# Performance work log

Measured on AMD Instinct MI355X. Metric: run time of the kernel, lower is better.

## Reference

```python
import jax, jax.numpy as jnp
import numpy as np

# SuperposedExpert: K parallel TT-factorized FFN paths + holographic routing.
# d_model=1024 factorized as [32,32]; d_ff=4096 as [64,64]; tt_ranks=[1,16,1] (r0/r2 squeezed).
K, D_MODEL, D_FF, RANK = 4, 1024, 4096, 16
IN1, IN2 = 32, 32          # factorize_for_tt(d_model)
F1, F2 = 64, 64            # factorize_for_tt(d_ff)
TEMP = 1.0                 # routing_temperature


def setup_inputs() -> dict:
    key = jax.random.key(0)
    ks = jax.random.split(key, 8)
    s = 0.05
    tokens = jax.random.normal(ks[0], (2048, D_MODEL), dtype=jnp.float32)
    # TT cores for ffn1: d_model -> d_ff  (input_dims [32,32], output_dims [64,64])
    ffn1_core1 = jax.random.normal(ks[1], (K, IN1, F1, RANK), dtype=jnp.float32) * s
    ffn1_core2 = jax.random.normal(ks[2], (K, RANK, IN2, F2), dtype=jnp.float32) * s
    # TT cores for ffn2: d_ff -> d_model (input_dims [64,64], output_dims [32,32])
    ffn2_core1 = jax.random.normal(ks[3], (K, F1, IN1, RANK), dtype=jnp.float32) * s
    ffn2_core2 = jax.random.normal(ks[4], (K, RANK, F2, IN2), dtype=jnp.float32) * s
    # Holographic routing params (hd_dim == d_model -> identity HD projection)
    pb = jax.random.normal(ks[5], (K, D_MODEL), dtype=jnp.float32)
    path_bases = pb / jnp.linalg.norm(pb, axis=-1, keepdims=True)  # orthogonal-ish init
    path_weights = jax.random.normal(ks[6], (K, D_MODEL), dtype=jnp.float32) * s
    return {
        'tokens': tokens,
        'ffn1_core1': ffn1_core1, 'ffn1_core2': ffn1_core2,
        'ffn2_core1': ffn2_core1, 'ffn2_core2': ffn2_core2,
        'path_bases': path_bases, 'path_weights': path_weights,
    }


def reference(tokens, ffn1_core1, ffn1_core2, ffn2_core1, ffn2_core2,
              path_bases, path_weights):
    N = tokens.shape[0]
    # ---- K superposed TT-FFN paths ----
    x3 = tokens.reshape(N, IN1, IN2)  # [n, a, b]
    # TT matmul 1: y[x,y] = sum_{a,b,r} G1[a,x,r] G2[r,b,y] x[a,b]
    h = jnp.einsum('nab,kaxr,krby->knxy', x3, ffn1_core1, ffn1_core2)
    h = jax.nn.gelu(h.reshape(K, N, D_FF))  # quantum_activation stand-in
    h3 = h.reshape(K, N, F1, F2)
    y = jnp.einsum('knab,kaxr,krby->knxy', h3, ffn2_core1, ffn2_core2)
    y = y.reshape(K, N, D_MODEL)  # per-path outputs
    # ---- Holographic HD routing (hd_dim == d_model: identity projection) ----
    logits = jnp.einsum('nd,kd->nk', tokens, path_bases) / TEMP
    gates = jax.nn.softmax(logits, axis=-1)  # [n, k]
    # Collapse superposition: per-path elementwise HD modulation + gated sum
    out = jnp.einsum('knd,kd,nk->nd', y, 1.0 + path_weights, gates)
    return out
```

## Files before the change

### kernel.cpp

```cpp
#include <hip/hip_runtime.h>
#include <stdint.h>

#define GAS __attribute__((address_space(1)))
#define LAS __attribute__((address_space(3)))

typedef __attribute__((ext_vector_type(8))) short short8;
typedef __attribute__((ext_vector_type(16))) float f32x16;
typedef __attribute__((ext_vector_type(4))) float f32x4;

static constexpr int N_TOK = 2048;
static constexpr int DM    = 1024;
static constexpr int DF    = 4096;
static constexpr int KP    = 4;

__device__ inline unsigned short f2bf(float f) {
  union { float f; uint32_t u; } v; v.f = f;
  uint32_t u = v.u;
  u += 0x7FFFu + ((u >> 16) & 1u);
  return (unsigned short)(u >> 16);
}

__device__ inline uint32_t pk_bf(float lo, float hi) {
  union { float f; uint32_t u; } a, b; a.f = lo; b.f = hi;
  uint32_t ul = a.u + 0x7FFFu + ((a.u >> 16) & 1u);
  uint32_t uh = b.u + 0x7FFFu + ((b.u >> 16) & 1u);
  return (ul >> 16) | (uh & 0xFFFF0000u);
}

__device__ inline float gelu_gate(float v, float g) {
  float t0 = v * v;
  float u  = v * __builtin_fmaf(t0, -0.10294456f, -2.3022539f);
  float e  = __builtin_amdgcn_exp2f(u);
  float r  = __builtin_amdgcn_rcpf(1.0f + e);
  return v * g * r;
}

__device__ inline void gld16(const void* g, void* l) {
  __builtin_amdgcn_global_load_lds((const GAS void*)g, (LAS void*)l, 16, 0, 0);
}

__global__ __launch_bounds__(256) void setup_kernel(
    const float* __restrict__ tokens, const float* __restrict__ pb,
    const float* __restrict__ c11, const float* __restrict__ c12,
    const float* __restrict__ c21, const float* __restrict__ c22,
    float* __restrict__ gates, unsigned short* __restrict__ xb,
    unsigned short* __restrict__ w1t, unsigned short* __restrict__ w2t) {
  __shared__ __align__(16) float sh[17472];
  const int blk = blockIdx.x;
  const int t = threadIdx.x;
  if (blk < 1024) {
    const int k = blk >> 8, x = (blk >> 2) & 63, y0 = (blk & 3) * 16;
    float* s1  = sh;
    float* s2T = sh + 512;
    if (t < 128) {
      int a = t >> 2, rq = (t & 3) * 4;
      *(float4*)(s1 + a * 16 + rq) =
          *(const float4*)(c11 + (((size_t)(k * 32 + a)) * 64 + x) * 16 + rq);
    }
#pragma unroll
    for (int j = 0; j < 8; ++j) {
      int i = t + j * 256;
      int rb = i >> 2, yy0 = (i & 3) * 4;
      float4 v = *(const float4*)(c12 + (size_t)(k * 16) * 2048 + (size_t)rb * 64 + y0 + yy0);
      s2T[(yy0 + 0) * 524 + rb] = v.x;
      s2T[(yy0 + 1) * 524 + rb] = v.y;
      s2T[(yy0 + 2) * 524 + rb] = v.z;
      s2T[(yy0 + 3) * 524 + rb] = v.w;
    }
    __syncthreads();
    const int a = t >> 3, b0 = (t & 7) * 4;
    float4 s1q[4];
#pragma unroll
    for (int q = 0; q < 4; ++q) s1q[q] = *(const float4*)(s1 + a * 16 + q * 4);
    const float* a0s = (const float*)s1q;
    for (int y = 0; y < 16; ++y) {
      const float* s2y = s2T + y * 524;
      float4 acc = {0.f, 0.f, 0.f, 0.f};
#pragma unroll
      for (int r = 0; r < 16; ++r) {
        float cv = a0s[r];
        float4 bv = *(const float4*)(s2y + r * 32 + b0);
        acc.x = __builtin_fmaf(cv, bv.x, acc.x);
        acc.y = __builtin_fmaf(cv, bv.y, acc.y);
        acc.z = __builtin_fmaf(cv, bv.z, acc.z);
        acc.w = __builtin_fmaf(cv, bv.w, acc.w);
      }
      ushort4 o; o.x = f2bf(acc.x); o.y = f2bf(acc.y); o.z = f2bf(acc.z); o.w = f2bf(acc.w);
      *(ushort4*)(w1t + ((size_t)k * DF + x * 64 + y0 + y) * DM + t * 4) = o;
    }
  } else if (blk < 2048) {
    const int bb = blk - 1024;
    const int jj = bb & 3;
    const int rest = bb >> 2;
    const int k = rest >> 6, x = (rest >> 1) & 31, y0 = (rest & 1) * 16;
    float* s1  = sh;
    float* s2T = sh + 1024;
    {
      int a = t >> 2, rq = (t & 3) * 4;
      *(float4*)(s1 + a * 16 + rq) =
          *(const float4*)(c21 + (((size_t)(k * 64 + a)) * 32 + x) * 16 + rq);
    }
#pragma unroll
    for (int j = 0; j < 16; ++j) {
      int i = t + j * 256;
      int rb = i >> 2, yy0 = (i & 3) * 4;
      float4 v = *(const float4*)(c22 + (size_t)(k * 16) * 2048 + (size_t)rb * 32 + y0 + yy0);
      s2T[(yy0 + 0) * 1028 + rb] = v.x;
      s2T[(yy0 + 1) * 1028 + rb] = v.y;
      s2T[(yy0 + 2) * 1028 + rb] = v.z;
      s2T[(yy0 + 3) * 1028 + rb] = v.w;
    }
    __syncthreads();
    const int b0 = (t & 15) * 4;
    const int a = (t >> 4) + jj * 16;
    float4 s1q[4];
#pragma unroll
    for (int q = 0; q < 4; ++q) s1q[q] = *(const float4*)(s1 + a * 16 + q * 4);
    const float* a0s = (const float*)s1q;
    for (int y = 0; y < 16; ++y) {
      const float* s2y = s2T + y * 1028;
      float4 acc = {0.f, 0.f, 0.f, 0.f};
#pragma unroll
      for (int r = 0; r < 16; ++r) {
        float cv = a0s[r];
        float4 bv = *(const float4*)(s2y + r * 64 + b0);
        acc.x = __builtin_fmaf(cv, bv.x, acc.x);
        acc.y = __builtin_fmaf(cv, bv.y, acc.y);
        acc.z = __builtin_fmaf(cv, bv.z, acc.z);
        acc.w = __builtin_fmaf(cv, bv.w, acc.w);
      }
      ushort4 o; o.x = f2bf(acc.x); o.y = f2bf(acc.y); o.z = f2bf(acc.z); o.w = f2bf(acc.w);
      *(ushort4*)(w2t + ((size_t)k * DM + x * 32 + y0 + y) * DF + t * 4 + jj * 1024) = o;
    }
  } else {
    const int wave = t >> 6, lane = t & 63;
    const int n = (blk - 2048) * 4 + wave;
    float s0 = 0.f, s1v = 0.f, s2v = 0.f, s3v = 0.f;
    const float4* tr = (const float4*)(tokens + (size_t)n * DM);
#pragma unroll
    for (int j = 0; j < 4; ++j) {
      int idx = j * 64 + lane;
      float4 tv = tr[idx];
      ushort4 b;
      b.x = f2bf(tv.x); b.y = f2bf(tv.y); b.z = f2bf(tv.z); b.w = f2bf(tv.w);
      *(ushort4*)(xb + (size_t)n * DM + idx * 4) = b;
      float4 q;
      q = ((const float4*)(pb + 0 * DM))[idx]; s0  += tv.x*q.x + tv.y*q.y + tv.z*q.z + tv.w*q.w;
      q = ((const float4*)(pb + 1 * DM))[idx]; s1v += tv.x*q.x + tv.y*q.y + tv.z*q.z + tv.w*q.w;
      q = ((const float4*)(pb + 2 * DM))[idx]; s2v += tv.x*q.x + tv.y*q.y + tv.z*q.z + tv.w*q.w;
      q = ((const float4*)(pb + 3 * DM))[idx]; s3v += tv.x*q.x + tv.y*q.y + tv.z*q.z + tv.w*q.w;
    }
#pragma unroll
    for (int off = 32; off > 0; off >>= 1) {
      s0  += __shfl_xor(s0, off);
      s1v += __shfl_xor(s1v, off);
      s2v += __shfl_xor(s2v, off);
      s3v += __shfl_xor(s3v, off);
    }
    if (lane == 0) {
      float m = fmaxf(fmaxf(s0, s1v), fmaxf(s2v, s3v));
      float e0 = __expf(s0 - m), e1 = __expf(s1v - m), e2 = __expf(s2v - m), e3 = __expf(s3v - m);
      float inv = 1.0f / (e0 + e1 + e2 + e3);
      float4 g; g.x = e0 * inv; g.y = e1 * inv; g.z = e2 * inv; g.w = e3 * inv;
      *(float4*)(gates + n * 4) = g;
    }
  }
}

#define PH_SYNC(V) do { \
    asm volatile("s_waitcnt vmcnt(" #V ")" ::: "memory"); \
    __builtin_amdgcn_s_barrier(); \
    __builtin_amdgcn_sched_barrier(0); \
  } while (0)

#define G1_TILE(KT, BO, WO, V0, V1, V2) do { \
    const int kn_ = ((KT) + 1) * 64; \
    const bool st_ = (KT) < 15; \
     \
    PH_SYNC(V0); \
    if (st_) { const unsigned short* s_ = Wg + (size_t)srow * DM + kn_ + lch * 8; \
      gld16(s_, smem + (WO) + t * 16); gld16(s_ + 64 * DM, smem + (WO) + 8192 + t * 16); } \
    _Pragma("unroll") for (int fi = 0; fi < 4; ++fi) \
      _Pragma("unroll") for (int s = 0; s < 2; ++s) \
        af[fi][s] = *(const short8*)(smem + (BO) + aRowB + fi * 2048 + (cxor16 ^ (s * 64) ^ (fi * 32))); \
    _Pragma("unroll") for (int ti = 0; ti < 2; ++ti) \
      _Pragma("unroll") for (int s = 0; s < 2; ++s) \
        bf0[ti][s] = *(const short8*)(smem + (BO) + xRowB + ti * 2048 + (cxor16 ^ (s * 64) ^ wnx64 ^ (ti * 32))); \
    __builtin_amdgcn_s_setprio(1); \
    _Pragma("unroll") for (int fi = 0; fi < 4; ++fi) \
      _Pragma("unroll") for (int ti = 0; ti < 2; ++ti) { \
        acc[0][0][fi][ti] = __builtin_amdgcn_mfma_f32_16x16x32_bf16(af[fi][0], bf0[ti][0], acc[0][0][fi][ti], 0, 0, 0); \
        acc[0][0][fi][ti] = __builtin_amdgcn_mfma_f32_16x16x32_bf16(af[fi][1], bf0[ti][1], acc[0][0][fi][ti], 0, 0, 0); } \
    __builtin_amdgcn_s_setprio(0); \
     \
    PH_SYNC(V1); \
    if (st_) { const unsigned short* s_ = Xg + (size_t)srow * DM + kn_ + lch * 8; \
      gld16(s_, smem + (WO) + 32768 + t * 16); gld16(s_ + 64 * DM, smem + (WO) + 32768 + 8192 + t * 16); } \
    _Pragma("unroll") for (int ti = 0; ti < 2; ++ti) \
      _Pragma("unroll") for (int s = 0; s < 2; ++s) \
        bf1[ti][s] = *(const short8*)(smem + (BO) + xRowB + 16384 + ti * 2048 + (cxor16 ^ (s * 64) ^ wnx64 ^ (ti * 32))); \
    __builtin_amdgcn_s_setprio(1); \
    _Pragma("unroll") for (int fi = 0; fi < 4; ++fi) \
      _Pragma("unroll") for (int ti = 0; ti < 2; ++ti) { \
        acc[0][1][fi][ti] = __builtin_amdgcn_mfma_f32_16x16x32_bf16(af[fi][0], bf1[ti][0], acc[0][1][fi][ti], 0, 0, 0); \
        acc[0][1][fi][ti] = __builtin_amdgcn_mfma_f32_16x16x32_bf16(af[fi][1], bf1[ti][1], acc[0][1][fi][ti], 0, 0, 0); } \
    __builtin_amdgcn_s_setprio(0); \
     \
    PH_SYNC(V2); \
    if (st_) { const unsigned short* s_ = Xg + (size_t)(128 + srow) * DM + kn_ + lch * 8; \
      gld16(s_, smem + (WO) + 32768 + 16384 + t * 16); gld16(s_ + 64 * DM, smem + (WO) + 32768 + 16384 + 8192 + t * 16); } \
    _Pragma("unroll") for (int fi = 0; fi < 4; ++fi) \
      _Pragma("unroll") for (int s = 0; s < 2; ++s) \
        af[fi][s] = *(const short8*)(smem + (BO) + aRowB + 16384 + fi * 2048 + (cxor16 ^ (s * 64) ^ (fi * 32))); \
    __builtin_amdgcn_s_setprio(1); \
    _Pragma("unroll") for (int fi = 0; fi < 4; ++fi) \
      _Pragma("unroll") for (int ti = 0; ti < 2; ++ti) { \
        acc[1][1][fi][ti] = __builtin_amdgcn_mfma_f32_16x16x32_bf16(af[fi][0], bf1[ti][0], acc[1][1][fi][ti], 0, 0, 0); \
        acc[1][1][fi][ti] = __builtin_amdgcn_mfma_f32_16x16x32_bf16(af[fi][1], bf1[ti][1], acc[1][1][fi][ti], 0, 0, 0); } \
    __builtin_amdgcn_s_setprio(0); \
     \
    if (st_) { const unsigned short* s_ = Wg + (size_t)(128 + srow) * DM + kn_ + lch * 8; \
      gld16(s_, smem + (WO) + 16384 + t * 16); gld16(s_ + 64 * DM, smem + (WO) + 16384 + 8192 + t * 16); } \
    __builtin_amdgcn_s_setprio(1); \
    _Pragma("unroll") for (int fi = 0; fi < 4; ++fi) \
      _Pragma("unroll") for (int ti = 0; ti < 2; ++ti) { \
        acc[1][0][fi][ti] = __builtin_amdgcn_mfma_f32_16x16x32_bf16(af[fi][0], bf0[ti][0], acc[1][0][fi][ti], 0, 0, 0); \
        acc[1][0][fi][ti] = __builtin_amdgcn_mfma_f32_16x16x32_bf16(af[fi][1], bf0[ti][1], acc[1][0][fi][ti], 0, 0, 0); } \
    __builtin_amdgcn_s_setprio(0); \
  } while (0)

__global__ __launch_bounds__(512, 1) void gemm1(
    const unsigned short* __restrict__ xb, const unsigned short* __restrict__ w1t,
    const float* __restrict__ gates, unsigned short* __restrict__ hg) {
  __shared__ __align__(16) char smem[131072];
  const int t = threadIdx.x, lane = t & 63, wv = t >> 6;
  const int wm = wv >> 2, wn = wv & 3;
  const int hw = blockIdx.x + (blockIdx.y << 3) + (blockIdx.z << 7);
  const int lg = (hw & 7) * 64 + (hw >> 3);
  const int m0 = (lg & 7) * 256;
  const int f0 = ((lg >> 3) & 15) * 256;
  const int kp = lg >> 7;
  const unsigned short* __restrict__ Wg = w1t + (size_t)kp * DF * DM + (size_t)f0 * DM;
  const unsigned short* __restrict__ Xg = xb + (size_t)m0 * DM;

  const int srow = t >> 3;
  const int lch  = (t & 7) ^ (srow & 7) ^ (srow >> 3);
  const int l15 = lane & 15, kg = lane >> 4;
  const int cxor16 = (kg ^ (lane & 7) ^ (l15 >> 3)) * 16;
  const int wnx64  = (wn & 1) * 64;
  const int aRowB  = (wm * 64 + l15) * 128;
  const int xRowB  = 32768 + (wn * 32 + l15) * 128;

  f32x4 acc[2][2][4][2] = {};
  short8 af[4][2], bf0[2][2], bf1[2][2];

  {
    const unsigned short* sw = Wg + (size_t)srow * DM + lch * 8;
    const unsigned short* sx = Xg + (size_t)srow * DM + lch * 8;
    gld16(sw,            smem + t * 16);
    gld16(sw + 64 * DM,  smem + 8192 + t * 16);
    gld16(sx,            smem + 32768 + t * 16);
    gld16(sx + 64 * DM,  smem + 32768 + 8192 + t * 16);
    gld16(sx + 128 * DM, smem + 32768 + 16384 + t * 16);
    gld16(sx + 192 * DM, smem + 32768 + 16384 + 8192 + t * 16);
    gld16(sw + 128 * DM, smem + 16384 + t * 16);
    gld16(sw + 192 * DM, smem + 16384 + 8192 + t * 16);
  }

#pragma unroll 1
  for (int kt = 0; kt < 14; kt += 2) {
    G1_TILE(kt,     0,     65536, 4, 4, 4);
    G1_TILE(kt + 1, 65536, 0,     4, 4, 4);
  }
  G1_TILE(14, 0,     65536, 4, 4, 4);
  G1_TILE(15, 65536, 0,     4, 2, 0);

  unsigned short* __restrict__ H = hg + (size_t)kp * N_TOK * DF;
#pragma unroll
  for (int cB = 0; cB < 2; ++cB)
#pragma unroll
    for (int ti = 0; ti < 2; ++ti) {
      const int tok = m0 + cB * 128 + wn * 32 + ti * 16 + l15;
      const float g = gates[tok * 4 + kp];
      unsigned short* hrow = H + (size_t)tok * DF + f0 + wm * 64 + kg * 4;
#pragma unroll
      for (int rA = 0; rA < 2; ++rA)
#pragma unroll
        for (int fi = 0; fi < 4; ++fi) {
          f32x4 v = acc[rA][cB][fi][ti];
          float r0 = gelu_gate(v.x, g);
          float r1 = gelu_gate(v.y, g);
          float r2 = gelu_gate(v.z, g);
          float r3 = gelu_gate(v.w, g);
          uint2 p; p.x = pk_bf(r0, r1); p.y = pk_bf(r2, r3);
          *(uint2*)(hrow + rA * 128 + fi * 16) = p;
        }
    }
}

#define G2_TILE(KT, BO, WO, V0, V1, V2) do { \
    const int kn_ = ((KT) + 1) * 64; \
    const bool st_ = (KT) < 63; \
     \
    PH_SYNC(V0); \
    if (st_) gld16(Wg + (size_t)srow * DF + kn_ + lch * 8, smem + (WO) + t * 16); \
    _Pragma("unroll") for (int fi = 0; fi < 2; ++fi) \
      _Pragma("unroll") for (int s = 0; s < 2; ++s) \
        af[fi][s] = *(const short8*)(smem + (BO) + awRowB + fi * 2048 + (cxor16 ^ awx ^ (fi * 32) ^ (s * 64))); \
    _Pragma("unroll") for (int ti = 0; ti < 2; ++ti) \
      _Pragma("unroll") for (int s = 0; s < 2; ++s) \
        bf0[ti][s] = *(const short8*)(smem + (BO) + xRowB + ti * 2048 + (cxor16 ^ wnx64 ^ (ti * 32) ^ (s * 64))); \
    __builtin_amdgcn_s_setprio(1); \
    _Pragma("unroll") for (int fi = 0; fi < 2; ++fi) \
      _Pragma("unroll") for (int ti = 0; ti < 2; ++ti) { \
        acc[0][0][fi][ti] = __builtin_amdgcn_mfma_f32_16x16x32_bf16(af[fi][0], bf0[ti][0], acc[0][0][fi][ti], 0, 0, 0); \
        acc[0][0][fi][ti] = __builtin_amdgcn_mfma_f32_16x16x32_bf16(af[fi][1], bf0[ti][1], acc[0][0][fi][ti], 0, 0, 0); } \
    __builtin_amdgcn_s_setprio(0); \
     \
    PH_SYNC(V1); \
    if (st_) { const unsigned short* s_ = Xg + (size_t)srow * DF + kn_ + lch * 8; \
      gld16(s_, smem + (WO) + 16384 + t * 16); gld16(s_ + 64 * DF, smem + (WO) + 16384 + 8192 + t * 16); } \
    _Pragma("unroll") for (int ti = 0; ti < 2; ++ti) \
      _Pragma("unroll") for (int s = 0; s < 2; ++s) \
        bf1[ti][s] = *(const short8*)(smem + (BO) + xRowB + 16384 + ti * 2048 + (cxor16 ^ wnx64 ^ (ti * 32) ^ (s * 64))); \
    __builtin_amdgcn_s_setprio(1); \
    _Pragma("unroll") for (int fi = 0; fi < 2; ++fi) \
      _Pragma("unroll") for (int ti = 0; ti < 2; ++ti) { \
        acc[0][1][fi][ti] = __builtin_amdgcn_mfma_f32_16x16x32_bf16(af[fi][0], bf1[ti][0], acc[0][1][fi][ti], 0, 0, 0); \
        acc[0][1][fi][ti] = __builtin_amdgcn_mfma_f32_16x16x32_bf16(af[fi][1], bf1[ti][1], acc[0][1][fi][ti], 0, 0, 0); } \
    __builtin_amdgcn_s_setprio(0); \
     \
    PH_SYNC(V2); \
    if (st_) { const unsigned short* s_ = Xg + (size_t)(128 + srow) * DF + kn_ + lch * 8; \
      gld16(s_, smem + (WO) + 32768 + t * 16); gld16(s_ + 64 * DF, smem + (WO) + 32768 + 8192 + t * 16); } \
    _Pragma("unroll") for (int fi = 0; fi < 2; ++fi) \
      _Pragma("unroll") for (int s = 0; s < 2; ++s) \
        af[fi][s] = *(const short8*)(smem + (BO) + awRowB + 8192 + fi * 2048 + (cxor16 ^ awx ^ (fi * 32) ^ (s * 64))); \
    __builtin_amdgcn_s_setprio(1); \
    _Pragma("unroll") for (int fi = 0; fi < 2; ++fi) \
      _Pragma("unroll") for (int ti = 0; ti < 2; ++ti) { \
        acc[1][1][fi][ti] = __builtin_amdgcn_mfma_f32_16x16x32_bf16(af[fi][0], bf1[ti][0], acc[1][1][fi][ti], 0, 0, 0); \
        acc[1][1][fi][ti] = __builtin_amdgcn_mfma_f32_16x16x32_bf16(af[fi][1], bf1[ti][1], acc[1][1][fi][ti], 0, 0, 0); } \
    __builtin_amdgcn_s_setprio(0); \
     \
    if (st_) gld16(Wg + (size_t)(64 + srow) * DF + kn_ + lch * 8, smem + (WO) + 8192 + t * 16); \
    __builtin_amdgcn_s_setprio(1); \
    _Pragma("unroll") for (int fi = 0; fi < 2; ++fi) \
      _Pragma("unroll") for (int ti = 0; ti < 2; ++ti) { \
        acc[1][0][fi][ti] = __builtin_amdgcn_mfma_f32_16x16x32_bf16(af[fi][0], bf0[ti][0], acc[1][0][fi][ti], 0, 0, 0); \
        acc[1][0][fi][ti] = __builtin_amdgcn_mfma_f32_16x16x32_bf16(af[fi][1], bf0[ti][1], acc[1][0][fi][ti], 0, 0, 0); } \
    __builtin_amdgcn_s_setprio(0); \
  } while (0)

__global__ __launch_bounds__(512, 1) void gemm2(
    const unsigned short* __restrict__ hg, const unsigned short* __restrict__ w2t,
    const float* __restrict__ pw, float* __restrict__ part) {
  __shared__ __align__(16) char smem[98304];
  const int t = threadIdx.x, lane = t & 63, wv = t >> 6;
  const int wm = wv >> 2, wn = wv & 3;
  const int hw = blockIdx.x + (blockIdx.y << 3) + (blockIdx.z << 6);
  const int lg = (hw & 7) * 32 + (hw >> 3);
  const int m0 = (lg & 7) * 256;
  const int n0 = ((lg >> 3) & 7) * 128;
  const int kp = lg >> 6;
  const unsigned short* __restrict__ Wg = w2t + (size_t)kp * DM * DF + (size_t)n0 * DF;
  const unsigned short* __restrict__ Xg = hg + (size_t)kp * N_TOK * DF + (size_t)m0 * DF;

  const int srow = t >> 3;
  const int lch  = (t & 7) ^ (srow & 7) ^ (srow >> 3);
  const int l15 = lane & 15, kg = lane >> 4;
  const int cxor16 = (kg ^ (lane & 7) ^ (l15 >> 3)) * 16;
  const int wnx64  = (wn & 1) * 64;
  const int awx    = wm * 64;
  const int awRowB = (wm * 32 + l15) * 128;
  const int xRowB  = 16384 + (wn * 32 + l15) * 128;

  f32x4 acc[2][2][2][2] = {};
  short8 af[2][2], bf0[2][2], bf1[2][2];

  {
    const unsigned short* sw = Wg + (size_t)srow * DF + lch * 8;
    const unsigned short* sx = Xg + (size_t)srow * DF + lch * 8;
    gld16(sw,            smem + t * 16);
    gld16(sx,            smem + 16384 + t * 16);
    gld16(sx + 64 * DF,  smem + 16384 + 8192 + t * 16);
    gld16(sx + 128 * DF, smem + 32768 + t * 16);
    gld16(sx + 192 * DF, smem + 32768 + 8192 + t * 16);
    gld16(sw + 64 * DF,  smem + 8192 + t * 16);
  }

#pragma unroll 1
  for (int kt = 0; kt < 62; kt += 2) {
    G2_TILE(kt,     0,     49152, 3, 2, 3);
    G2_TILE(kt + 1, 49152, 0,     3, 2, 3);
  }
  G2_TILE(62, 0,     49152, 3, 2, 3);
  G2_TILE(63, 49152, 0,     3, 1, 0);

  float* __restrict__ P = part + (size_t)kp * N_TOK * DM;
  float4 pwv[2][2];
#pragma unroll
  for (int rA = 0; rA < 2; ++rA)
#pragma unroll
    for (int fi = 0; fi < 2; ++fi) {
      float4 w = *(const float4*)(pw + kp * DM + n0 + rA * 64 + wm * 32 + fi * 16 + kg * 4);
      pwv[rA][fi].x = 1.0f + w.x; pwv[rA][fi].y = 1.0f + w.y;
      pwv[rA][fi].z = 1.0f + w.z; pwv[rA][fi].w = 1.0f + w.w;
    }
#pragma unroll
  for (int cB = 0; cB < 2; ++cB)
#pragma unroll
    for (int ti = 0; ti < 2; ++ti) {
      const int tok = m0 + cB * 128 + wn * 32 + ti * 16 + l15;
      float* prow = P + (size_t)tok * DM + n0 + wm * 32 + kg * 4;
#pragma unroll
      for (int rA = 0; rA < 2; ++rA)
#pragma unroll
        for (int fi = 0; fi < 2; ++fi) {
          f32x4 v = acc[rA][cB][fi][ti];
          float4 o;
          o.x = pwv[rA][fi].x * v.x;
          o.y = pwv[rA][fi].y * v.y;
          o.z = pwv[rA][fi].z * v.z;
          o.w = pwv[rA][fi].w * v.w;
          *(float4*)(prow + rA * 64 + fi * 16) = o;
        }
    }
}

__global__ __launch_bounds__(256) void reduce_k(
    const float* __restrict__ part, float* __restrict__ out) {
  const size_t i = ((size_t)blockIdx.x * 256 + threadIdx.x) * 4;
  const size_t S = (size_t)N_TOK * DM;
  float4 a = *(const float4*)(part + i);
  float4 b = *(const float4*)(part + S + i);
  float4 c = *(const float4*)(part + 2 * S + i);
  float4 d = *(const float4*)(part + 3 * S + i);
  float4 r;
  r.x = a.x + b.x + c.x + d.x;
  r.y = a.y + b.y + c.y + d.y;
  r.z = a.z + b.z + c.z + d.z;
  r.w = a.w + b.w + c.w + d.w;
  *(float4*)(out + i) = r;
}

extern "C" void kernel_launch(void* const* d_in, const int* in_sizes, int n_in,
                              void* d_out, int out_size, void* d_ws, size_t ws_size,
                              hipStream_t stream) {
  const float* tokens = (const float*)d_in[0];
  const float* f1c1   = (const float*)d_in[1];
  const float* f1c2   = (const float*)d_in[2];
  const float* f2c1   = (const float*)d_in[3];
  const float* f2c2   = (const float*)d_in[4];
  const float* pb     = (const float*)d_in[5];
  const float* pw     = (const float*)d_in[6];
  float* out = (float*)d_out;

  char* ws = (char*)d_ws;
  unsigned short* xb  = (unsigned short*)(ws);
  unsigned short* w1t = (unsigned short*)(ws + (4ull  << 20));
  float*          part = (float*)(ws + (4ull << 20));
  unsigned short* w2t = (unsigned short*)(ws + (36ull << 20));
  unsigned short* hg  = (unsigned short*)(ws + (68ull << 20));
  float*          gates = (float*)(ws + (132ull << 20));

  hipLaunchKernelGGL(setup_kernel, dim3(2560), dim3(256), 0, stream,
                     tokens, pb, f1c1, f1c2, f2c1, f2c2, gates, xb, w1t, w2t);
  hipLaunchKernelGGL(gemm1, dim3(8, 16, KP), dim3(512), 0, stream, xb, w1t, gates, hg);
  hipLaunchKernelGGL(gemm2, dim3(8, 8, KP), dim3(512), 0, stream, hg, w2t, pw, part);
  hipLaunchKernelGGL(reduce_k, dim3(2048), dim3(256), 0, stream, part, out);
}
```

Measured before the change: 244.9 us.

## Shrink GEMM tiles to 128x128 with 4-wave blocks and shared tile macro

```diff
diff --git a/kernel.cpp b/kernel.cpp
--- a/kernel.cpp
+++ b/kernel.cpp
@@ -173,229 +173,163 @@
     __builtin_amdgcn_sched_barrier(0); \
   } while (0)
 
-#define G1_TILE(KT, BO, WO, V0, V1, V2) do { \
-    const int kn_ = ((KT) + 1) * 64; \
-    const bool st_ = (KT) < 15; \
-     \
-    PH_SYNC(V0); \
-    if (st_) { const unsigned short* s_ = Wg + (size_t)srow * DM + kn_ + lch * 8; \
-      gld16(s_, smem + (WO) + t * 16); gld16(s_ + 64 * DM, smem + (WO) + 8192 + t * 16); } \
-    _Pragma("unroll") for (int fi = 0; fi < 4; ++fi) \
-      _Pragma("unroll") for (int s = 0; s < 2; ++s) \
-        af[fi][s] = *(const short8*)(smem + (BO) + aRowB + fi * 2048 + (cxor16 ^ (s * 64) ^ (fi * 32))); \
-    _Pragma("unroll") for (int ti = 0; ti < 2; ++ti) \
-      _Pragma("unroll") for (int s = 0; s < 2; ++s) \
-        bf0[ti][s] = *(const short8*)(smem + (BO) + xRowB + ti * 2048 + (cxor16 ^ (s * 64) ^ wnx64 ^ (ti * 32))); \
-    __builtin_amdgcn_s_setprio(1); \
-    _Pragma("unroll") for (int fi = 0; fi < 4; ++fi) \
-      _Pragma("unroll") for (int ti = 0; ti < 2; ++ti) { \
-        acc[0][0][fi][ti] = __builtin_amdgcn_mfma_f32_16x16x32_bf16(af[fi][0], bf0[ti][0], acc[0][0][fi][ti], 0, 0, 0); \
-        acc[0][0][fi][ti] = __builtin_amdgcn_mfma_f32_16x16x32_bf16(af[fi][1], bf0[ti][1], acc[0][0][fi][ti], 0, 0, 0); } \
-    __builtin_amdgcn_s_setprio(0); \
-     \
-    PH_SYNC(V1); \
-    if (st_) { const unsigned short* s_ = Xg + (size_t)srow * DM + kn_ + lch * 8; \
-      gld16(s_, smem + (WO) + 32768 + t * 16); gld16(s_ + 64 * DM, smem + (WO) + 32768 + 8192 + t * 16); } \
-    _Pragma("unroll") for (int ti = 0; ti < 2; ++ti) \
-      _Pragma("unroll") for (int s = 0; s < 2; ++s) \
-        bf1[ti][s] = *(const short8*)(smem + (BO) + xRowB + 16384 + ti * 2048 + (cxor16 ^ (s * 64) ^ wnx64 ^ (ti * 32))); \
-    __builtin_amdgcn_s_setprio(1); \
-    _Pragma("unroll") for (int fi = 0; fi < 4; ++fi) \
-      _Pragma("unroll") for (int ti = 0; ti < 2; ++ti) { \
-        acc[0][1][fi][ti] = __builtin_amdgcn_mfma_f32_16x16x32_bf16(af[fi][0], bf1[ti][0], acc[0][1][fi][ti], 0, 0, 0); \
-        acc[0][1][fi][ti] = __builtin_amdgcn_mfma_f32_16x16x32_bf16(af[fi][1], bf1[ti][1], acc[0][1][fi][ti], 0, 0, 0); } \
-    __builtin_amdgcn_s_setprio(0); \
-     \
-    PH_SYNC(V2); \
-    if (st_) { const unsigned short* s_ = Xg + (size_t)(128 + srow) * DM + kn_ + lch * 8; \
-      gld16(s_, smem + (WO) + 32768 + 16384 + t * 16); gld16(s_ + 64 * DM, smem + (WO) + 32768 + 16384 + 8192 + t * 16); } \
-    _Pragma("unroll") for (int fi = 0; fi < 4; ++fi) \
-      _Pragma("unroll") for (int s = 0; s < 2; ++s) \
-        af[fi][s] = *(const short8*)(smem + (BO) + aRowB + 16384 + fi * 2048 + (cxor16 ^ (s * 64) ^ (fi * 32))); \
-    __builtin_amdgcn_s_setprio(1); \
-    _Pragma("unroll") for (int fi = 0; fi < 4; ++fi) \
-      _Pragma("unroll") for (int ti = 0; ti < 2; ++ti) { \
-        acc[1][1][fi][ti] = __builtin_amdgcn_mfma_f32_16x16x32_bf16(af[fi][0], bf1[ti][0], acc[1][1][fi][ti], 0, 0, 0); \
-        acc[1][1][fi][ti] = __builtin_amdgcn_mfma_f32_16x16x32_bf16(af[fi][1], bf1[ti][1], acc[1][1][fi][ti], 0, 0, 0); } \
-    __builtin_amdgcn_s_setprio(0); \
-     \
-    if (st_) { const unsigned short* s_ = Wg + (size_t)(128 + srow) * DM + kn_ + lch * 8; \
-      gld16(s_, smem + (WO) + 16384 + t * 16); gld16(s_ + 64 * DM, smem + (WO) + 16384 + 8192 + t * 16); } \
-    __builtin_amdgcn_s_setprio(1); \
-    _Pragma("unroll") for (int fi = 0; fi < 4; ++fi) \
-      _Pragma("unroll") for (int ti = 0; ti < 2; ++ti) { \
-        acc[1][0][fi][ti] = __builtin_amdgcn_mfma_f32_16x16x32_bf16(af[fi][0], bf0[ti][0], acc[1][0][fi][ti], 0, 0, 0); \
-        acc[1][0][fi][ti] = __builtin_amdgcn_mfma_f32_16x16x32_bf16(af[fi][1], bf0[ti][1], acc[1][0][fi][ti], 0, 0, 0); } \
-    __builtin_amdgcn_s_setprio(0); \
-  } while (0)
-
-__global__ __launch_bounds__(512, 1) void gemm1(
+#define MFMA8(ACCQ, AFR, BFR) do { \
+  __builtin_amdgcn_s_setprio(1); \
+  _Pragma("unroll") for (int fi = 0; fi < 2; ++fi) \
+    _Pragma("unroll") for (int ti = 0; ti < 2; ++ti) { \
+      ACCQ[fi][ti] = __builtin_amdgcn_mfma_f32_16x16x32_bf16(AFR[fi][0], BFR[ti][0], ACCQ[fi][ti], 0, 0, 0); \
+      ACCQ[fi][ti] = __builtin_amdgcn_mfma_f32_16x16x32_bf16(AFR[fi][1], BFR[ti][1], ACCQ[fi][ti], 0, 0, 0); } \
+  __builtin_amdgcn_s_setprio(0); \
+} while (0)
+
+#define GTILE(KT, BO, WO, V0, V1, V2, LIMIT, STR) do { \
+  const int kn_ = ((KT) + 1) * 64; \
+  const bool st_ = (KT) < (LIMIT); \
+   \
+  PH_SYNC(V0); \
+  if (st_) { \
+    gld16(Wg + (size_t)srow * (STR) + kn_ + lch * 8,        smem + (WO) + t * 16); \
+    gld16(Wg + (size_t)(64 + srow) * (STR) + kn_ + lch * 8, smem + (WO) + 4096 + t * 16); } \
+  _Pragma("unroll") for (int fi = 0; fi < 2; ++fi) \
+    _Pragma("unroll") for (int s = 0; s < 2; ++s) \
+      af[fi][s] = *(const short8*)(smem + (BO) + aB + fi * 2048 + (((s * 4) ^ cx ^ (fi * 2)) & 7) * 16); \
+  _Pragma("unroll") for (int ti = 0; ti < 2; ++ti) \
+    _Pragma("unroll") for (int s = 0; s < 2; ++s) \
+      bf0[ti][s] = *(const short8*)(smem + (BO) + xB + ti * 2048 + (((s * 4) ^ cx ^ (ti * 2)) & 7) * 16); \
+  MFMA8(acc[0][0], af, bf0); \
+   \
+  PH_SYNC(V1); \
+  if (st_) { \
+    gld16(Xg + (size_t)srow * (STR) + kn_ + lch * 8,        smem + (WO) + 16384 + t * 16); \
+    gld16(Xg + (size_t)(64 + srow) * (STR) + kn_ + lch * 8, smem + (WO) + 16384 + 4096 + t * 16); } \
+  _Pragma("unroll") for (int ti = 0; ti < 2; ++ti) \
+    _Pragma("unroll") for (int s = 0; s < 2; ++s) \
+      bf1[ti][s] = *(const short8*)(smem + (BO) + xB + 8192 + ti * 2048 + (((s * 4) ^ cx ^ (ti * 2)) & 7) * 16); \
+  MFMA8(acc[0][1], af, bf1); \
+   \
+  PH_SYNC(V2); \
+  if (st_) { \
+    gld16(Xg + (size_t)(32 + srow) * (STR) + kn_ + lch * 8, smem + (WO) + 24576 + t * 16); \
+    gld16(Xg + (size_t)(96 + srow) * (STR) + kn_ + lch * 8, smem + (WO) + 24576 + 4096 + t * 16); } \
+  _Pragma("unroll") for (int fi = 0; fi < 2; ++fi) \
+    _Pragma("unroll") for (int s = 0; s < 2; ++s) \
+      af[fi][s] = *(const short8*)(smem + (BO) + aB + 8192 + fi * 2048 + (((s * 4) ^ cx ^ (fi * 2)) & 7) * 16); \
+  MFMA8(acc[1][1], af, bf1); \
+   \
+  if (st_) { \
+    gld16(Wg + (size_t)(32 + srow) * (STR) + kn_ + lch * 8, smem + (WO) + 8192 + t * 16); \
+    gld16(Wg + (size_t)(96 + srow) * (STR) + kn_ + lch * 8, smem + (WO) + 8192 + 4096 + t * 16); } \
+  MFMA8(acc[1][0], af, bf0); \
+} while (0)
+
+__global__ __launch_bounds__(256) void gemm1(
     const unsigned short* __restrict__ xb, const unsigned short* __restrict__ w1t,
     const float* __restrict__ gates, unsigned short* __restrict__ hg) {
-  __shared__ __align__(16) char smem[131072];
+  __shared__ __align__(16) char smem[65536];
   const int t = threadIdx.x, lane = t & 63, wv = t >> 6;
-  const int wm = wv >> 2, wn = wv & 3;
-  const int hw = blockIdx.x + (blockIdx.y << 3) + (blockIdx.z << 7);
-  const int lg = (hw & 7) * 64 + (hw >> 3);
-  const int m0 = (lg & 7) * 256;
-  const int f0 = ((lg >> 3) & 15) * 256;
-  const int kp = lg >> 7;
+  const int wm = wv >> 1, wn = wv & 1;
+  const int hw = blockIdx.x + (blockIdx.y << 4) + (blockIdx.z << 9);
+  const int lg = (hw & 7) * 256 + (hw >> 3);
+  const int m0 = (lg & 15) * 128;
+  const int f0 = ((lg >> 4) & 31) * 128;
+  const int kp = lg >> 9;
   const unsigned short* __restrict__ Wg = w1t + (size_t)kp * DF * DM + (size_t)f0 * DM;
   const unsigned short* __restrict__ Xg = xb + (size_t)m0 * DM;
 
   const int srow = t >> 3;
   const int lch  = (t & 7) ^ (srow & 7) ^ (srow >> 3);
   const int l15 = lane & 15, kg = lane >> 4;
-  const int cxor16 = (kg ^ (lane & 7) ^ (l15 >> 3)) * 16;
-  const int wnx64  = (wn & 1) * 64;
-  const int aRowB  = (wm * 64 + l15) * 128;
-  const int xRowB  = 32768 + (wn * 32 + l15) * 128;
-
-  f32x4 acc[2][2][4][2] = {};
-  short8 af[4][2], bf0[2][2], bf1[2][2];
+  const int cx  = kg ^ (l15 & 7) ^ (l15 >> 3);
+  const int aB  = wm * 4096 + l15 * 128;
+  const int xB  = 16384 + wn * 4096 + l15 * 128;
+
+  f32x4 acc[2][2][2][2] = {};
+  short8 af[2][2], bf0[2][2], bf1[2][2];
 
   {
-    const unsigned short* sw = Wg + (size_t)srow * DM + lch * 8;
-    const unsigned short* sx = Xg + (size_t)srow * DM + lch * 8;
-    gld16(sw,            smem + t * 16);
-    gld16(sw + 64 * DM,  smem + 8192 + t * 16);
-    gld16(sx,            smem + 32768 + t * 16);
-    gld16(sx + 64 * DM,  smem + 32768 + 8192 + t * 16);
-    gld16(sx + 128 * DM, smem + 32768 + 16384 + t * 16);
-    gld16(sx + 192 * DM, smem + 32768 + 16384 + 8192 + t * 16);
-    gld16(sw + 128 * DM, smem + 16384 + t * 16);
-    gld16(sw + 192 * DM, smem + 16384 + 8192 + t * 16);
+    gld16(Wg + (size_t)srow * DM + lch * 8,        smem + t * 16);
+    gld16(Wg + (size_t)(64 + srow) * DM + lch * 8, smem + 4096 + t * 16);
+    gld16(Xg + (size_t)srow * DM + lch * 8,        smem + 16384 + t * 16);
+    gld16(Xg + (size_t)(64 + srow) * DM + lch * 8, smem + 16384 + 4096 + t * 16);
+    gld16(Xg + (size_t)(32 + srow) * DM + lch * 8, smem + 24576 + t * 16);
+    gld16(Xg + (size_t)(96 + srow) * DM + lch * 8, smem + 24576 + 4096 + t * 16);
+    gld16(Wg + (size_t)(32 + srow) * DM + lch * 8, smem + 8192 + t * 16);
+    gld16(Wg + (size_t)(96 + srow) * DM + lch * 8, smem + 8192 + 4096 + t * 16);
   }
 
 #pragma unroll 1
   for (int kt = 0; kt < 14; kt += 2) {
-    G1_TILE(kt,     0,     65536, 4, 4, 4);
-    G1_TILE(kt + 1, 65536, 0,     4, 4, 4);
+    GTILE(kt,     0,     32768, 4, 4, 4, 15, DM);
+    GTILE(kt + 1, 32768, 0,     4, 4, 4, 15, DM);
   }
-  G1_TILE(14, 0,     65536, 4, 4, 4);
-  G1_TILE(15, 65536, 0,     4, 2, 0);
+  GTILE(14, 0,     32768, 4, 4, 4, 15, DM);
+  GTILE(15, 32768, 0,     4, 2, 0, 15, DM);
 
   unsigned short* __restrict__ H = hg + (size_t)kp * N_TOK * DF;
 #pragma unroll
   for (int cB = 0; cB < 2; ++cB)
 #pragma unroll
     for (int ti = 0; ti < 2; ++ti) {
-      const int tok = m0 + cB * 128 + wn * 32 + ti * 16 + l15;
+      const int tok = m0 + wn * 64 + cB * 32 + ti * 16 + l15;
       const float g = gates[tok * 4 + kp];
       unsigned short* hrow = H + (size_t)tok * DF + f0 + wm * 64 + kg * 4;
 #pragma unroll
       for (int rA = 0; rA < 2; ++rA)
 #pragma unroll
-        for (int fi = 0; fi < 4; ++fi) {
+        for (int fi = 0; fi < 2; ++fi) {
           f32x4 v = acc[rA][cB][fi][ti];
           float r0 = gelu_gate(v.x, g);
           float r1 = gelu_gate(v.y, g);
           float r2 = gelu_gate(v.z, g);
           float r3 = gelu_gate(v.w, g);
           uint2 p; p.x = pk_bf(r0, r1); p.y = pk_bf(r2, r3);
-          *(uint2*)(hrow + rA * 128 + fi * 16) = p;
+          *(uint2*)(hrow + rA * 32 + fi * 16) = p;
         }
     }
 }
 
-#define G2_TILE(KT, BO, WO, V0, V1, V2) do { \
-    const int kn_ = ((KT) + 1) * 64; \
-    const bool st_ = (KT) < 63; \
-     \
-    PH_SYNC(V0); \
-    if (st_) gld16(Wg + (size_t)srow * DF + kn_ + lch * 8, smem + (WO) + t * 16); \
-    _Pragma("unroll") for (int fi = 0; fi < 2; ++fi) \
-      _Pragma("unroll") for (int s = 0; s < 2; ++s) \
-        af[fi][s] = *(const short8*)(smem + (BO) + awRowB + fi * 2048 + (cxor16 ^ awx ^ (fi * 32) ^ (s * 64))); \
-    _Pragma("unroll") for (int ti = 0; ti < 2; ++ti) \
-      _Pragma("unroll") for (int s = 0; s < 2; ++s) \
-        bf0[ti][s] = *(const short8*)(smem + (BO) + xRowB + ti * 2048 + (cxor16 ^ wnx64 ^ (ti * 32) ^ (s * 64))); \
-    __builtin_amdgcn_s_setprio(1); \
-    _Pragma("unroll") for (int fi = 0; fi < 2; ++fi) \
-      _Pragma("unroll") for (int ti = 0; ti < 2; ++ti) { \
-        acc[0][0][fi][ti] = __builtin_amdgcn_mfma_f32_16x16x32_bf16(af[fi][0], bf0[ti][0], acc[0][0][fi][ti], 0, 0, 0); \
-        acc[0][0][fi][ti] = __builtin_amdgcn_mfma_f32_16x16x32_bf16(af[fi][1], bf0[ti][1], acc[0][0][fi][ti], 0, 0, 0); } \
-    __builtin_amdgcn_s_setprio(0); \
-     \
-    PH_SYNC(V1); \
-    if (st_) { const unsigned short* s_ = Xg + (size_t)srow * DF + kn_ + lch * 8; \
-      gld16(s_, smem + (WO) + 16384 + t * 16); gld16(s_ + 64 * DF, smem + (WO) + 16384 + 8192 + t * 16); } \
-    _Pragma("unroll") for (int ti = 0; ti < 2; ++ti) \
-      _Pragma("unroll") for (int s = 0; s < 2; ++s) \
-        bf1[ti][s] = *(const short8*)(smem + (BO) + xRowB + 16384 + ti * 2048 + (cxor16 ^ wnx64 ^ (ti * 32) ^ (s * 64))); \
-    __builtin_amdgcn_s_setprio(1); \
-    _Pragma("unroll") for (int fi = 0; fi < 2; ++fi) \
-      _Pragma("unroll") for (int ti = 0; ti < 2; ++ti) { \
-        acc[0][1][fi][ti] = __builtin_amdgcn_mfma_f32_16x16x32_bf16(af[fi][0], bf1[ti][0], acc[0][1][fi][ti], 0, 0, 0); \
-        acc[0][1][fi][ti] = __builtin_amdgcn_mfma_f32_16x16x32_bf16(af[fi][1], bf1[ti][1], acc[0][1][fi][ti], 0, 0, 0); } \
-    __builtin_amdgcn_s_setprio(0); \
-     \
-    PH_SYNC(V2); \
-    if (st_) { const unsigned short* s_ = Xg + (size_t)(128 + srow) * DF + kn_ + lch * 8; \
-      gld16(s_, smem + (WO) + 32768 + t * 16); gld16(s_ + 64 * DF, smem + (WO) + 32768 + 8192 + t * 16); } \
-    _Pragma("unroll") for (int fi = 0; fi < 2; ++fi) \
-      _Pragma("unroll") for (int s = 0; s < 2; ++s) \
-        af[fi][s] = *(const short8*)(smem + (BO) + awRowB + 8192 + fi * 2048 + (cxor16 ^ awx ^ (fi * 32) ^ (s * 64))); \
-    __builtin_amdgcn_s_setprio(1); \
-    _Pragma("unroll") for (int fi = 0; fi < 2; ++fi) \
-      _Pragma("unroll") for (int ti = 0; ti < 2; ++ti) { \
-        acc[1][1][fi][ti] = __builtin_amdgcn_mfma_f32_16x16x32_bf16(af[fi][0], bf1[ti][0], acc[1][1][fi][ti], 0, 0, 0); \
-        acc[1][1][fi][ti] = __builtin_amdgcn_mfma_f32_16x16x32_bf16(af[fi][1], bf1[ti][1], acc[1][1][fi][ti], 0, 0, 0); } \
-    __builtin_amdgcn_s_setprio(0); \
-     \
-    if (st_) gld16(Wg + (size_t)(64 + srow) * DF + kn_ + lch * 8, smem + (WO) + 8192 + t * 16); \
-    __builtin_amdgcn_s_setprio(1); \
-    _Pragma("unroll") for (int fi = 0; fi < 2; ++fi) \
-      _Pragma("unroll") for (int ti = 0; ti < 2; ++ti) { \
-        acc[1][0][fi][ti] = __builtin_amdgcn_mfma_f32_16x16x32_bf16(af[fi][0], bf0[ti][0], acc[1][0][fi][ti], 0, 0, 0); \
-        acc[1][0][fi][ti] = __builtin_amdgcn_mfma_f32_16x16x32_bf16(af[fi][1], bf0[ti][1], acc[1][0][fi][ti], 0, 0, 0); } \
-    __builtin_amdgcn_s_setprio(0); \
-  } while (0)
-
-__global__ __launch_bounds__(512, 1) void gemm2(
+__global__ __launch_bounds__(256) void gemm2(
     const unsigned short* __restrict__ hg, const unsigned short* __restrict__ w2t,
     const float* __restrict__ pw, float* __restrict__ part) {
-  __shared__ __align__(16) char smem[98304];
+  __shared__ __align__(16) char smem[65536];
   const int t = threadIdx.x, lane = t & 63, wv = t >> 6;
-  const int wm = wv >> 2, wn = wv & 3;
-  const int hw = blockIdx.x + (blockIdx.y << 3) + (blockIdx.z << 6);
-  const int lg = (hw & 7) * 32 + (hw >> 3);
-  const int m0 = (lg & 7) * 256;
-  const int n0 = ((lg >> 3) & 7) * 128;
-  const int kp = lg >> 6;
+  const int wm = wv >> 1, wn = wv & 1;
+  const int hw = blockIdx.x + (blockIdx.y << 4) + (blockIdx.z << 7);
+  const int lg = (hw & 7) * 64 + (hw >> 3);
+  const int m0 = (lg & 15) * 128;
+  const int n0 = ((lg >> 4) & 7) * 128;
+  const int kp = lg >> 7;
   const unsigned short* __restrict__ Wg = w2t + (size_t)kp * DM * DF + (size_t)n0 * DF;
   const unsigned short* __restrict__ Xg = hg + (size_t)kp * N_TOK * DF + (size_t)m0 * DF;
 
   const int srow = t >> 3;
   const int lch  = (t & 7) ^ (srow & 7) ^ (srow >> 3);
   const int l15 = lane & 15, kg = lane >> 4;
-  const int cxor16 = (kg ^ (lane & 7) ^ (l15 >> 3)) * 16;
-  const int wnx64  = (wn & 1) * 64;
-  const int awx    = wm * 64;
-  const int awRowB = (wm * 32 + l15) * 128;
-  const int xRowB  = 16384 + (wn * 32 + l15) * 128;
+  const int cx  = kg ^ (l15 & 7) ^ (l15 >> 3);
+  const int aB  = wm * 4096 + l15 * 128;
+  const int xB  = 16384 + wn * 4096 + l15 * 128;
 
   f32x4 acc[2][2][2][2] = {};
   short8 af[2][2], bf0[2][2], bf1[2][2];
 
   {
-    const unsigned short* sw = Wg + (size_t)srow * DF + lch * 8;
-    const unsigned short* sx = Xg + (size_t)srow * DF + lch * 8;
-    gld16(sw,            smem + t * 16);
-    gld16(sx,            smem + 16384 + t * 16);
-    gld16(sx + 64 * DF,  smem + 16384 + 8192 + t * 16);
-    gld16(sx + 128 * DF, smem + 32768 + t * 16);
-    gld16(sx + 192 * DF, smem + 32768 + 8192 + t * 16);
-    gld16(sw + 64 * DF,  smem + 8192 + t * 16);
+    gld16(Wg + (size_t)srow * DF + lch * 8,        smem + t * 16);
+    gld16(Wg + (size_t)(64 + srow) * DF + lch * 8, smem + 4096 + t * 16);
+    gld16(Xg + (size_t)srow * DF + lch * 8,        smem + 16384 + t * 16);
+    gld16(Xg + (size_t)(64 + srow) * DF + lch * 8, smem + 16384 + 4096 + t * 16);
+    gld16(Xg + (size_t)(32 + srow) * DF + lch * 8, smem + 24576 + t * 16);
+    gld16(Xg + (size_t)(96 + srow) * DF + lch * 8, smem + 24576 + 4096 + t * 16);
+    gld16(Wg + (size_t)(32 + srow) * DF + lch * 8, smem + 8192 + t * 16);
+    gld16(Wg + (size_t)(96 + srow) * DF + lch * 8, smem + 8192 + 4096 + t * 16);
   }
 
 #pragma unroll 1
   for (int kt = 0; kt < 62; kt += 2) {
-    G2_TILE(kt,     0,     49152, 3, 2, 3);
-    G2_TILE(kt + 1, 49152, 0,     3, 2, 3);
+    GTILE(kt,     0,     32768, 4, 4, 4, 63, DF);
+    GTILE(kt + 1, 32768, 0,     4, 4, 4, 63, DF);
   }
-  G2_TILE(62, 0,     49152, 3, 2, 3);
-  G2_TILE(63, 49152, 0,     3, 1, 0);
+  GTILE(62, 0,     32768, 4, 4, 4, 63, DF);
+  GTILE(63, 32768, 0,     4, 2, 0, 63, DF);
 
   float* __restrict__ P = part + (size_t)kp * N_TOK * DM;
   float4 pwv[2][2];
@@ -403,7 +337,7 @@
   for (int rA = 0; rA < 2; ++rA)
 #pragma unroll
     for (int fi = 0; fi < 2; ++fi) {
-      float4 w = *(const float4*)(pw + kp * DM + n0 + rA * 64 + wm * 32 + fi * 16 + kg * 4);
+      float4 w = *(const float4*)(pw + kp * DM + n0 + wm * 64 + rA * 32 + fi * 16 + kg * 4);
       pwv[rA][fi].x = 1.0f + w.x; pwv[rA][fi].y = 1.0f + w.y;
       pwv[rA][fi].z = 1.0f + w.z; pwv[rA][fi].w = 1.0f + w.w;
     }
@@ -411,8 +345,8 @@
   for (int cB = 0; cB < 2; ++cB)
 #pragma unroll
     for (int ti = 0; ti < 2; ++ti) {
-      const int tok = m0 + cB * 128 + wn * 32 + ti * 16 + l15;
-      float* prow = P + (size_t)tok * DM + n0 + wm * 32 + kg * 4;
+      const int tok = m0 + wn * 64 + cB * 32 + ti * 16 + l15;
+      float* prow = P + (size_t)tok * DM + n0 + wm * 64 + kg * 4;
 #pragma unroll
       for (int rA = 0; rA < 2; ++rA)
 #pragma unroll
@@ -423,7 +357,7 @@
           o.y = pwv[rA][fi].y * v.y;
           o.z = pwv[rA][fi].z * v.z;
           o.w = pwv[rA][fi].w * v.w;
-          *(float4*)(prow + rA * 64 + fi * 16) = o;
+          *(float4*)(prow + rA * 32 + fi * 16) = o;
         }
     }
 }
@@ -466,7 +400,7 @@
 
   hipLaunchKernelGGL(setup_kernel, dim3(2560), dim3(256), 0, stream,
                      tokens, pb, f1c1, f1c2, f2c1, f2c2, gates, xb, w1t, w2t);
-  hipLaunchKernelGGL(gemm1, dim3(8, 16, KP), dim3(512), 0, stream, xb, w1t, gates, hg);
-  hipLaunchKernelGGL(gemm2, dim3(8, 8, KP), dim3(512), 0, stream, hg, w2t, pw, part);
+  hipLaunchKernelGGL(gemm1, dim3(16, 32, KP), dim3(256), 0, stream, xb, w1t, gates, hg);
+  hipLaunchKernelGGL(gemm2, dim3(16, 8, KP), dim3(256), 0, stream, hg, w2t, pw, part);
   hipLaunchKernelGGL(reduce_k, dim3(2048), dim3(256), 0, stream, part, out);
 }
```

Measured after the change: 265.8 us. +8.5%, slower.
